# Optimization experiments

Hardware: AMD Instinct MI355X
Metric: run time of the kernel (lower is better)

The kernel has to match this reference:

```python
import jax, jax.numpy as jnp
import numpy as np

NEG_INF = float("-inf")
WINDOW = 5  # window_size in LocalAttention; half = WINDOW // 2 = 2


def setup_inputs() -> dict:
    key = jax.random.key(0)
    kq, kk, kv = jax.random.split(key, 3)
    B, L, H, E = 4, 2048, 8, 64
    queries = jax.random.normal(kq, (B, L, H, E), dtype=jnp.float32)
    keys = jax.random.normal(kk, (B, L, H, E), dtype=jnp.float32)
    values = jax.random.normal(kv, (B, L, H, E), dtype=jnp.float32)
    return {"queries": queries, "keys": keys, "values": values}


def reference(queries, keys, values):
    # queries/keys/values: [B, L, H, E]; dropout is identity (eval mode).
    B, L, H, E = queries.shape
    scale = 1.0 / jnp.sqrt(jnp.asarray(E, dtype=queries.dtype))
    # Shared scores for both branches: [B, H, L, S]
    scores = jnp.einsum("blhe,bshe->bhls", queries, keys)

    # Global (unmasked) branch
    A_global = jax.nn.softmax(scale * scores, axis=-1)

    # Local branch: torch mask allows j in [max(i-2,0), min(i+2,L)) => i-2 <= j <= i+1
    half = WINDOW // 2
    i = jnp.arange(L)[:, None]
    j = jnp.arange(L)[None, :]
    allowed = (j - i >= -half) & (j - i < half)  # [L, L], asymmetric window
    local_scores = jnp.where(allowed, scores, NEG_INF)
    A_local = jax.nn.softmax(scale * local_scores, axis=-1)

    # Sum of the two attention outputs == (A_global + A_local) @ V
    out = jnp.einsum("bhls,bshd->blhd", A_global + A_local, values)
    return out
```

## Files before the change

### kernel.cpp

```cpp
#include <hip/hip_runtime.h>
#include <hip/hip_bf16.h>
#include <stdint.h>


#define LQ 2048
#define HQ 8
#define EQ 64
#define BQ 4
#define BM 64
#define BN 64
#define RS (HQ * EQ)
#define SCALE_LOG2E 0.18033688011112042f
#define NTILE (LQ / BN)
#define TILE_U32 2048
#define IMG_U32 (BQ * HQ * NTILE * TILE_U32)

typedef __attribute__((ext_vector_type(8))) short bf16x8;
typedef __attribute__((ext_vector_type(4))) float f32x4;
typedef __attribute__((ext_vector_type(4))) unsigned int u32x4;
typedef __attribute__((ext_vector_type(2))) unsigned int u32x2;

static __device__ __forceinline__ unsigned int pk2(float lo, float hi) {
    union { float f; unsigned int u; } a, b; a.f = lo; b.f = hi;
    return ((a.u + 0x8000u) >> 16) | ((b.u + 0x8000u) & 0xffff0000u);
}
static __device__ __forceinline__ float fexp2(float x) {
    float r;
    asm volatile("v_exp_f32 %0, %1\n\ts_nop 1" : "=v"(r) : "v"(x));
    return r;
}
static __device__ __forceinline__ void gload16(const uint32_t* g, void* l) {
    __builtin_amdgcn_global_load_lds(
        (const __attribute__((address_space(1))) unsigned int*)g,
        (__attribute__((address_space(3))) unsigned int*)l, 16, 0, 0);
}

__global__ __launch_bounds__(256) void prepack_kernel(
    const float* __restrict__ K, const float* __restrict__ V,
    uint32_t* __restrict__ Kimg, uint32_t* __restrict__ Vimg)
{
    const int tid = threadIdx.x;
    const int jc  = blockIdx.x;
    const int bh  = blockIdx.y;
    const int b   = bh >> 3;
    const int h   = bh & 7;
    const int j0  = jc * BN;
    const float* Kbh = K + (size_t)b * LQ * RS + h * EQ;
    const float* Vbh = V + (size_t)b * LQ * RS + h * EQ;
    uint32_t* Kt = Kimg + (size_t)(bh * NTILE + jc) * TILE_U32;
    uint32_t* Vt = Vimg + (size_t)(bh * NTILE + jc) * TILE_U32;

    #pragma unroll
    for (int it = 0; it < 2; ++it) {
        int t2 = tid + it * 256;
        int jr = t2 >> 3, eo = t2 & 7;
        const float* src = Kbh + (size_t)(j0 + jr) * RS + eo * 8;
        float4 a  = *(const float4*)src;
        float4 bv = *(const float4*)(src + 4);
        u32x4 p;
        p.x = pk2(a.x, a.y);   p.y = pk2(a.z, a.w);
        p.z = pk2(bv.x, bv.y); p.w = pk2(bv.z, bv.w);
        *(u32x4*)&Kt[jr * 32 + ((eo ^ (jr & 7)) << 2)] = p;
    }
    #pragma unroll
    for (int it = 0; it < 2; ++it) {
        int t2 = tid + it * 256;
        int e = t2 & 63, jo = t2 >> 6;
        const float* src = Vbh + (size_t)(j0 + jo * 8) * RS + e;
        float v0 = src[0 * RS], v1 = src[1 * RS], v2 = src[2 * RS], v3 = src[3 * RS];
        float v4 = src[4 * RS], v5 = src[5 * RS], v6 = src[6 * RS], v7 = src[7 * RS];
        u32x4 p;
        p.x = pk2(v0, v1); p.y = pk2(v2, v3);
        p.z = pk2(v4, v5); p.w = pk2(v6, v7);
        *(u32x4*)&Vt[e * 32 + ((jo ^ (e & 7)) << 2)] = p;
    }
}

__global__ __launch_bounds__(128, 2) void hybrid_attn_v5(
    const float* __restrict__ Q, const float* __restrict__ K,
    const float* __restrict__ V, const uint32_t* __restrict__ Kimg,
    const uint32_t* __restrict__ Vimg, float* __restrict__ O)
{
    __shared__ unsigned short KV[8192];
    __shared__ unsigned short Pt[2][2048];
    __shared__ float sloc[BM][4];

    const int tid  = threadIdx.x;
    const int wave = tid >> 6;
    const int lane = tid & 63;
    const int c    = lane & 15;
    const int g    = lane >> 4;
    const int qt   = blockIdx.x;
    const int bh   = blockIdx.y;
    const int b    = bh >> 3;
    const int h    = bh & 7;
    const int i0   = qt * BM;
    const int c7   = c & 7;
    const int sw3  = c7 << 1;

    const float* Qbh = Q + (size_t)b * LQ * RS + h * EQ;
    const float* Kbh = K + (size_t)b * LQ * RS + h * EQ;
    const float* Vbh = V + (size_t)b * LQ * RS + h * EQ;
    float*       Obh = O + (size_t)b * LQ * RS + h * EQ;

    bf16x8 qf[2][2];
    #pragma unroll
    for (int t = 0; t < 2; ++t) {
        const int iq = i0 + wave * 32 + t * 16 + c;
        const float* qrow = Qbh + (size_t)iq * RS + g * 8;
        #pragma unroll
        for (int f = 0; f < 2; ++f) {
            float4 a  = *(const float4*)(qrow + f * 32);
            float4 bv = *(const float4*)(qrow + f * 32 + 4);
            union { bf16x8 v; unsigned int u[4]; } fr;
            fr.u[0] = pk2(a.x  * SCALE_LOG2E, a.y  * SCALE_LOG2E);
            fr.u[1] = pk2(a.z  * SCALE_LOG2E, a.w  * SCALE_LOG2E);
            fr.u[2] = pk2(bv.x * SCALE_LOG2E, bv.y * SCALE_LOG2E);
            fr.u[3] = pk2(bv.z * SCALE_LOG2E, bv.w * SCALE_LOG2E);
            qf[t][f] = fr.v;
        }
    }

    const int fo0 = c * 64 + ((g ^ c7) << 3);
    const int fo1 = c * 64 + (((4 | g) ^ c7) << 3);

    unsigned short* pw[4];
    #pragma unroll
    for (int n = 0; n < 4; ++n)
        pw[n] = &Pt[wave][c * 64 + ((((n << 2) | g) ^ sw3) << 2)];
    unsigned short* pr0 = &Pt[wave][c * 64 + (((g << 1) ^ sw3) << 2)];
    unsigned short* pr1 = &Pt[wave][c * 64 + (((8 | (g << 1)) ^ sw3) << 2)];

    const uint32_t* kgb = Kimg + (size_t)bh * (NTILE * TILE_U32) + wave * 1024 + lane * 4;
    const uint32_t* vgb = Vimg + (size_t)bh * (NTILE * TILE_U32) + wave * 1024 + lane * 4;

    f32x4 oacc[2][4];
    #pragma unroll
    for (int t = 0; t < 2; ++t)
        #pragma unroll
        for (int eg = 0; eg < 4; ++eg) oacc[t][eg] = (f32x4){0.f, 0.f, 0.f, 0.f};
    float lsum[2] = {0.f, 0.f};

    for (int jc = 0; jc < NTILE; ++jc) {
        __syncthreads();
        const uint32_t* kg = kgb + (size_t)jc * TILE_U32;
        const uint32_t* vg = vgb + (size_t)jc * TILE_U32;
        #pragma unroll
        for (int kk = 0; kk < 4; ++kk)
            gload16(kg + kk * 256, &KV[wave * 2048 + kk * 512]);
        #pragma unroll
        for (int kk = 0; kk < 4; ++kk)
            gload16(vg + kk * 256, &KV[4096 + wave * 2048 + kk * 512]);
        __syncthreads();

        bf16x8 kfr[4][2];
        #pragma unroll
        for (int n = 0; n < 4; ++n) {
            kfr[n][0] = *(const bf16x8*)&KV[n * 1024 + fo0];
            kfr[n][1] = *(const bf16x8*)&KV[n * 1024 + fo1];
        }

        #pragma unroll
        for (int t = 0; t < 2; ++t) {
            f32x4 sf[4];
            #pragma unroll
            for (int n = 0; n < 4; ++n) {
                f32x4 acc = (f32x4){0.f, 0.f, 0.f, 0.f};
                acc = __builtin_amdgcn_mfma_f32_16x16x32_bf16(kfr[n][0], qf[t][0], acc, 0, 0, 0);
                acc = __builtin_amdgcn_mfma_f32_16x16x32_bf16(kfr[n][1], qf[t][1], acc, 0, 0, 0);
                sf[n] = acc;
            }
            float ls = 0.f;
            #pragma unroll
            for (int n = 0; n < 4; ++n) {
                float p0 = fexp2(sf[n][0]);
                float p1 = fexp2(sf[n][1]);
                float p2 = fexp2(sf[n][2]);
                float p3 = fexp2(sf[n][3]);
                ls += (p0 + p1) + (p2 + p3);
                u32x2 pkd;
                pkd.x = pk2(p0, p1);
                pkd.y = pk2(p2, p3);
                *(u32x2*)(pw[n] + t * 1024) = pkd;
            }
            lsum[t] += ls;
        }
        asm volatile("s_waitcnt lgkmcnt(0)" ::: "memory");

        bf16x8 pfr[2][2];
        #pragma unroll
        for (int t = 0; t < 2; ++t) {
            pfr[t][0] = *(const bf16x8*)(pr0 + t * 1024);
            pfr[t][1] = *(const bf16x8*)(pr1 + t * 1024);
        }
        #pragma unroll
        for (int eg = 0; eg < 4; ++eg) {
            bf16x8 v0 = *(const bf16x8*)&KV[4096 + eg * 1024 + fo0];
            bf16x8 v1 = *(const bf16x8*)&KV[4096 + eg * 1024 + fo1];
            #pragma unroll
            for (int t = 0; t < 2; ++t) {
                oacc[t][eg] = __builtin_amdgcn_mfma_f32_16x16x32_bf16(v0, pfr[t][0], oacc[t][eg], 0, 0, 0);
                oacc[t][eg] = __builtin_amdgcn_mfma_f32_16x16x32_bf16(v1, pfr[t][1], oacc[t][eg], 0, 0, 0);
            }
        }
    }

    float linv[2];
    #pragma unroll
    for (int t = 0; t < 2; ++t) {
        float l = lsum[t];
        l += __shfl_xor(l, 16);
        l += __shfl_xor(l, 32);
        linv[t] = 1.0f / l;
    }

    {
        const int br = tid >> 1;
        const int i  = i0 + br;
        const float* qrow = Qbh + (size_t)i * RS;
        #pragma unroll
        for (int halfj = 0; halfj < 2; ++halfj) {
            const int jj = (tid & 1) * 2 + halfj;
            const int j  = i - 2 + jj;
            float s = -INFINITY;
            if (j >= 0 && j < LQ) {
                const float* krow = Kbh + (size_t)j * RS;
                float acc = 0.f;
                #pragma unroll
                for (int e = 0; e < 64; e += 4) {
                    float4 qa = *(const float4*)(qrow + e);
                    float4 ka = *(const float4*)(krow + e);
                    acc = fmaf(qa.x, ka.x, acc); acc = fmaf(qa.y, ka.y, acc);
                    acc = fmaf(qa.z, ka.z, acc); acc = fmaf(qa.w, ka.w, acc);
                }
                s = 0.125f * acc;
            }
            sloc[br][jj] = s;
        }
    }
    __syncthreads();

    #pragma unroll
    for (int t = 0; t < 2; ++t) {
        const int row = wave * 32 + t * 16 + c;
        const int i   = i0 + row;
        float s0 = sloc[row][0], s1 = sloc[row][1], s2 = sloc[row][2], s3 = sloc[row][3];
        float mx = fmaxf(fmaxf(s0, s1), fmaxf(s2, s3));
        float w0 = expf(s0 - mx), w1 = expf(s1 - mx);
        float w2 = expf(s2 - mx), w3 = expf(s3 - mx);
        float inv = 1.0f / (w0 + w1 + w2 + w3);
        w0 *= inv; w1 *= inv; w2 *= inv; w3 *= inv;
        const float li = linv[t];
        float* orow = Obh + (size_t)i * RS;
        #pragma unroll
        for (int eg = 0; eg < 4; ++eg) {
            const int e0 = eg * 16 + g * 4;
            float v0 = oacc[t][eg][0] * li;
            float v1 = oacc[t][eg][1] * li;
            float v2 = oacc[t][eg][2] * li;
            float v3 = oacc[t][eg][3] * li;
            if (w0 > 0.f) {
                float4 vv = *(const float4*)(Vbh + (size_t)(i - 2) * RS + e0);
                v0 = fmaf(w0, vv.x, v0); v1 = fmaf(w0, vv.y, v1);
                v2 = fmaf(w0, vv.z, v2); v3 = fmaf(w0, vv.w, v3);
            }
            if (w1 > 0.f) {
                float4 vv = *(const float4*)(Vbh + (size_t)(i - 1) * RS + e0);
                v0 = fmaf(w1, vv.x, v0); v1 = fmaf(w1, vv.y, v1);
                v2 = fmaf(w1, vv.z, v2); v3 = fmaf(w1, vv.w, v3);
            }
            {
                float4 vv = *(const float4*)(Vbh + (size_t)i * RS + e0);
                v0 = fmaf(w2, vv.x, v0); v1 = fmaf(w2, vv.y, v1);
                v2 = fmaf(w2, vv.z, v2); v3 = fmaf(w2, vv.w, v3);
            }
            if (w3 > 0.f) {
                float4 vv = *(const float4*)(Vbh + (size_t)(i + 1) * RS + e0);
                v0 = fmaf(w3, vv.x, v0); v1 = fmaf(w3, vv.y, v1);
                v2 = fmaf(w3, vv.z, v2); v3 = fmaf(w3, vv.w, v3);
            }
            float4 outv; outv.x = v0; outv.y = v1; outv.z = v2; outv.w = v3;
            *(float4*)(orow + e0) = outv;
        }
    }
}

__global__ __launch_bounds__(256) void hybrid_attn_fb(
    const float* __restrict__ Q, const float* __restrict__ K,
    const float* __restrict__ V, float* __restrict__ O)
{
    __shared__ unsigned short Ks[64 * 64];
    __shared__ unsigned short Vt[64 * 64];
    __shared__ unsigned short Ps[4][16 * 64];
    __shared__ float sloc[BM][4];

    const int tid  = threadIdx.x;
    const int wave = tid >> 6;
    const int lane = tid & 63;
    const int c    = lane & 15;
    const int g    = lane >> 4;
    const int qt   = blockIdx.x;
    const int bh   = blockIdx.y;
    const int b    = bh >> 3;
    const int h    = bh & 7;
    const int i0   = qt * BM;

    const float* Qbh = Q + (size_t)b * LQ * RS + h * EQ;
    const float* Kbh = K + (size_t)b * LQ * RS + h * EQ;
    const float* Vbh = V + (size_t)b * LQ * RS + h * EQ;
    float*       Obh = O + (size_t)b * LQ * RS + h * EQ;

    bf16x8 qf[2];
    {
        const int iA = i0 + wave * 16 + c;
        const float* qrow = Qbh + (size_t)iA * RS + g * 8;
        #pragma unroll
        for (int f = 0; f < 2; ++f) {
            float4 a  = *(const float4*)(qrow + f * 32);
            float4 bv = *(const float4*)(qrow + f * 32 + 4);
            union { bf16x8 v; unsigned int u[4]; } fr;
            fr.u[0] = pk2(a.x  * SCALE_LOG2E, a.y  * SCALE_LOG2E);
            fr.u[1] = pk2(a.z  * SCALE_LOG2E, a.w  * SCALE_LOG2E);
            fr.u[2] = pk2(bv.x * SCALE_LOG2E, bv.y * SCALE_LOG2E);
            fr.u[3] = pk2(bv.z * SCALE_LOG2E, bv.w * SCALE_LOG2E);
            qf[f] = fr.v;
        }
    }

    int kfo[4][2], vfo[4][2], pfo[2], pso[4][4];
    #pragma unroll
    for (int n = 0; n < 4; ++n)
        #pragma unroll
        for (int f = 0; f < 2; ++f)
            kfo[n][f] = (n * 16 + c) * 64 + ((((f << 2) | g) ^ (c & 7)) << 3);
    #pragma unroll
    for (int eg = 0; eg < 4; ++eg)
        #pragma unroll
        for (int kh = 0; kh < 2; ++kh)
            vfo[eg][kh] = (eg * 16 + c) * 64 + ((((kh << 2) | g) ^ (c & 7)) << 3);
    #pragma unroll
    for (int kh = 0; kh < 2; ++kh)
        pfo[kh] = c * 64 + ((((kh << 2) | g) ^ (c & 7)) << 3);
    #pragma unroll
    for (int r = 0; r < 4; ++r) {
        const int row = g * 4 + r;
        #pragma unroll
        for (int n = 0; n < 4; ++n) {
            const int col = n * 16 + c;
            pso[r][n] = row * 64 + ((((col >> 3) ^ (row & 7)) << 3) | (col & 7));
        }
    }

    f32x4 oacc[4];
    #pragma unroll
    for (int eg = 0; eg < 4; ++eg) oacc[eg] = (f32x4){0.f, 0.f, 0.f, 0.f};
    float l_r[4] = {0.f, 0.f, 0.f, 0.f};

    for (int j0 = 0; j0 < LQ; j0 += BN) {
        __syncthreads();
        #pragma unroll
        for (int it = 0; it < 2; ++it) {
            int t2 = tid + it * 256;
            int jr = t2 >> 3, eo = t2 & 7;
            const float* src = Kbh + (size_t)(j0 + jr) * RS + eo * 8;
            float4 a  = *(const float4*)src;
            float4 bv = *(const float4*)(src + 4);
            u32x4 p;
            p.x = pk2(a.x, a.y);   p.y = pk2(a.z, a.w);
            p.z = pk2(bv.x, bv.y); p.w = pk2(bv.z, bv.w);
            *(u32x4*)&Ks[jr * 64 + ((eo ^ (jr & 7)) << 3)] = p;
        }
        #pragma unroll
        for (int it = 0; it < 2; ++it) {
            int t2 = tid + it * 256;
            int e = t2 & 63, jo = t2 >> 6;
            const float* src = Vbh + (size_t)(j0 + jo * 8) * RS + e;
            float v0 = src[0 * RS], v1 = src[1 * RS], v2 = src[2 * RS], v3 = src[3 * RS];
            float v4 = src[4 * RS], v5 = src[5 * RS], v6 = src[6 * RS], v7 = src[7 * RS];
            u32x4 p;
            p.x = pk2(v0, v1); p.y = pk2(v2, v3);
            p.z = pk2(v4, v5); p.w = pk2(v6, v7);
            *(u32x4*)&Vt[e * 64 + ((jo ^ (e & 7)) << 3)] = p;
        }
        __syncthreads();

        f32x4 sf[4];
        #pragma unroll
        for (int n = 0; n < 4; ++n) {
            bf16x8 k0 = *(const bf16x8*)&Ks[kfo[n][0]];
            bf16x8 k1 = *(const bf16x8*)&Ks[kfo[n][1]];
            f32x4 acc = (f32x4){0.f, 0.f, 0.f, 0.f};
            acc = __builtin_amdgcn_mfma_f32_16x16x32_bf16(qf[0], k0, acc, 0, 0, 0);
            acc = __builtin_amdgcn_mfma_f32_16x16x32_bf16(qf[1], k1, acc, 0, 0, 0);
            sf[n] = acc;
        }
        #pragma unroll
        for (int r = 0; r < 4; ++r) {
            float p0 = fexp2(sf[0][r]);
            float p1 = fexp2(sf[1][r]);
            float p2 = fexp2(sf[2][r]);
            float p3 = fexp2(sf[3][r]);
            l_r[r] += (p0 + p1) + (p2 + p3);
            Ps[wave][pso[r][0]] = (unsigned short)(pk2(p0, 0.f) & 0xffff);
            Ps[wave][pso[r][1]] = (unsigned short)(pk2(p1, 0.f) & 0xffff);
            Ps[wave][pso[r][2]] = (unsigned short)(pk2(p2, 0.f) & 0xffff);
            Ps[wave][pso[r][3]] = (unsigned short)(pk2(p3, 0.f) & 0xffff);
        }
        asm volatile("s_waitcnt lgkmcnt(0)" ::: "memory");

        bf16x8 pf0 = *(const bf16x8*)&Ps[wave][pfo[0]];
        bf16x8 pf1 = *(const bf16x8*)&Ps[wave][pfo[1]];
        #pragma unroll
        for (int eg = 0; eg < 4; ++eg) {
            bf16x8 v0 = *(const bf16x8*)&Vt[vfo[eg][0]];
            bf16x8 v1 = *(const bf16x8*)&Vt[vfo[eg][1]];
            oacc[eg] = __builtin_amdgcn_mfma_f32_16x16x32_bf16(pf0, v0, oacc[eg], 0, 0, 0);
            oacc[eg] = __builtin_amdgcn_mfma_f32_16x16x32_bf16(pf1, v1, oacc[eg], 0, 0, 0);
        }
    }

    #pragma unroll
    for (int r = 0; r < 4; ++r) {
        float l = l_r[r];
        l += __shfl_xor(l, 1);
        l += __shfl_xor(l, 2);
        l += __shfl_xor(l, 4);
        l += __shfl_xor(l, 8);
        l_r[r] = 1.0f / l;
    }

    {
        const int br = tid >> 2;
        const int jj = tid & 3;
        const int i  = i0 + br;
        const int j  = i - 2 + jj;
        float s = -INFINITY;
        if (j >= 0 && j < LQ) {
            const float* qrow = Qbh + (size_t)i * RS;
            const float* krow = Kbh + (size_t)j * RS;
            float acc = 0.f;
            #pragma unroll
            for (int e = 0; e < 64; e += 4) {
                float4 qa = *(const float4*)(qrow + e);
                float4 ka = *(const float4*)(krow + e);
                acc = fmaf(qa.x, ka.x, acc); acc = fmaf(qa.y, ka.y, acc);
                acc = fmaf(qa.z, ka.z, acc); acc = fmaf(qa.w, ka.w, acc);
            }
            s = 0.125f * acc;
        }
        sloc[br][jj] = s;
    }
    __syncthreads();

    #pragma unroll
    for (int r = 0; r < 4; ++r) {
        const int row = wave * 16 + g * 4 + r;
        const int i   = i0 + row;
        float s0 = sloc[row][0], s1 = sloc[row][1], s2 = sloc[row][2], s3 = sloc[row][3];
        float mx = fmaxf(fmaxf(s0, s1), fmaxf(s2, s3));
        float w0 = expf(s0 - mx), w1 = expf(s1 - mx);
        float w2 = expf(s2 - mx), w3 = expf(s3 - mx);
        float inv = 1.0f / (w0 + w1 + w2 + w3);
        w0 *= inv; w1 *= inv; w2 *= inv; w3 *= inv;
        const float li = l_r[r];
        float* orow = Obh + (size_t)i * RS;
        #pragma unroll
        for (int eg = 0; eg < 4; ++eg) {
            const int e = eg * 16 + c;
            float val = oacc[eg][r] * li;
            if (w0 > 0.f) val += w0 * Vbh[(size_t)(i - 2) * RS + e];
            if (w1 > 0.f) val += w1 * Vbh[(size_t)(i - 1) * RS + e];
            if (w2 > 0.f) val += w2 * Vbh[(size_t)(i    ) * RS + e];
            if (w3 > 0.f) val += w3 * Vbh[(size_t)(i + 1) * RS + e];
            orow[e] = val;
        }
    }
}

extern "C" void kernel_launch(void* const* d_in, const int* in_sizes, int n_in,
                              void* d_out, int out_size, void* d_ws, size_t ws_size,
                              hipStream_t stream) {
    (void)in_sizes; (void)n_in; (void)out_size;
    const float* Q = (const float*)d_in[0];
    const float* K = (const float*)d_in[1];
    const float* V = (const float*)d_in[2];
    float* O = (float*)d_out;
    const size_t need = (size_t)2 * IMG_U32 * 4;
    if (ws_size >= need) {
        uint32_t* Kimg = (uint32_t*)d_ws;
        uint32_t* Vimg = Kimg + IMG_U32;
        hipLaunchKernelGGL(prepack_kernel, dim3(NTILE, BQ * HQ), dim3(256), 0, stream,
                           K, V, Kimg, Vimg);
        hipLaunchKernelGGL(hybrid_attn_v5, dim3(LQ / BM, BQ * HQ), dim3(128), 0, stream,
                           Q, K, V, Kimg, Vimg, O);
    } else {
        hipLaunchKernelGGL(hybrid_attn_fb, dim3(LQ / BM, BQ * HQ), dim3(256), 0, stream,
                           Q, K, V, O);
    }
}
```

Measured before the change: 163.6 us.

## Coalesce V prepack via LDS transpose and remap grid for XCD locality

The V prepack now reads rows with coalesced float4 loads into a padded LDS tile, converts to bf16 and transposes there, replacing the strided scalar column gathers. The main attention kernel uses a 1D grid whose block index is remapped so that consecutive blocks land on different batch-head pairs, likely so each XCD's L2 holds fewer distinct K/V images. The P bf16 conversion uses a simpler single-value helper. The changes add an LDS barrier in the prepack and depend on the hardware dispatch order for the locality benefit.

```diff
diff --git a/kernel.cpp b/kernel.cpp
--- a/kernel.cpp
+++ b/kernel.cpp
@@ -20,6 +20,10 @@
 typedef __attribute__((ext_vector_type(4))) unsigned int u32x4;
 typedef __attribute__((ext_vector_type(2))) unsigned int u32x2;
 
+static __device__ __forceinline__ unsigned int f2bf(float f) {
+    union { float f; unsigned int u; } c; c.f = f;
+    return (c.u + 0x8000u) >> 16;
+}
 static __device__ __forceinline__ unsigned int pk2(float lo, float hi) {
     union { float f; unsigned int u; } a, b; a.f = lo; b.f = hi;
     return ((a.u + 0x8000u) >> 16) | ((b.u + 0x8000u) & 0xffff0000u);
@@ -39,6 +43,8 @@
     const float* __restrict__ K, const float* __restrict__ V,
     uint32_t* __restrict__ Kimg, uint32_t* __restrict__ Vimg)
 {
+    __shared__ unsigned short vt[64 * 72];
+
     const int tid = threadIdx.x;
     const int jc  = blockIdx.x;
     const int bh  = blockIdx.y;
@@ -62,21 +68,33 @@
         p.z = pk2(bv.x, bv.y); p.w = pk2(bv.z, bv.w);
         *(u32x4*)&Kt[jr * 32 + ((eo ^ (jr & 7)) << 2)] = p;
     }
+
+    {
+        const int jr = tid >> 2;
+        const int e0 = (tid & 3) * 16;
+        const float* src = Vbh + (size_t)(j0 + jr) * RS + e0;
+        #pragma unroll
+        for (int q = 0; q < 4; ++q) {
+            float4 a = *(const float4*)(src + q * 4);
+            const int e = e0 + q * 4;
+            vt[(e + 0) * 72 + jr] = (unsigned short)f2bf(a.x);
+            vt[(e + 1) * 72 + jr] = (unsigned short)f2bf(a.y);
+            vt[(e + 2) * 72 + jr] = (unsigned short)f2bf(a.z);
+            vt[(e + 3) * 72 + jr] = (unsigned short)f2bf(a.w);
+        }
+    }
+    __syncthreads();
+
     #pragma unroll
     for (int it = 0; it < 2; ++it) {
-        int t2 = tid + it * 256;
-        int e = t2 & 63, jo = t2 >> 6;
-        const float* src = Vbh + (size_t)(j0 + jo * 8) * RS + e;
-        float v0 = src[0 * RS], v1 = src[1 * RS], v2 = src[2 * RS], v3 = src[3 * RS];
-        float v4 = src[4 * RS], v5 = src[5 * RS], v6 = src[6 * RS], v7 = src[7 * RS];
-        u32x4 p;
-        p.x = pk2(v0, v1); p.y = pk2(v2, v3);
-        p.z = pk2(v4, v5); p.w = pk2(v6, v7);
+        const int i  = tid + it * 256;
+        const int e  = i >> 3, jo = i & 7;
+        u32x4 p = *(const u32x4*)&vt[e * 72 + jo * 8];
         *(u32x4*)&Vt[e * 32 + ((jo ^ (e & 7)) << 2)] = p;
     }
 }
 
-__global__ __launch_bounds__(128, 2) void hybrid_attn_v5(
+__global__ __launch_bounds__(128, 2) void hybrid_attn_v7(
     const float* __restrict__ Q, const float* __restrict__ K,
     const float* __restrict__ V, const uint32_t* __restrict__ Kimg,
     const uint32_t* __restrict__ Vimg, float* __restrict__ O)
@@ -90,8 +108,9 @@
     const int lane = tid & 63;
     const int c    = lane & 15;
     const int g    = lane >> 4;
-    const int qt   = blockIdx.x;
-    const int bh   = blockIdx.y;
+    const int id   = blockIdx.x;
+    const int bh   = (id & 7) * 4 + ((id >> 3) & 3);
+    const int qt   = id >> 5;
     const int b    = bh >> 3;
     const int h    = bh & 7;
     const int i0   = qt * BM;
@@ -401,10 +420,10 @@
             float p2 = fexp2(sf[2][r]);
             float p3 = fexp2(sf[3][r]);
             l_r[r] += (p0 + p1) + (p2 + p3);
-            Ps[wave][pso[r][0]] = (unsigned short)(pk2(p0, 0.f) & 0xffff);
-            Ps[wave][pso[r][1]] = (unsigned short)(pk2(p1, 0.f) & 0xffff);
-            Ps[wave][pso[r][2]] = (unsigned short)(pk2(p2, 0.f) & 0xffff);
-            Ps[wave][pso[r][3]] = (unsigned short)(pk2(p3, 0.f) & 0xffff);
+            Ps[wave][pso[r][0]] = (unsigned short)f2bf(p0);
+            Ps[wave][pso[r][1]] = (unsigned short)f2bf(p1);
+            Ps[wave][pso[r][2]] = (unsigned short)f2bf(p2);
+            Ps[wave][pso[r][3]] = (unsigned short)f2bf(p3);
         }
         asm volatile("s_waitcnt lgkmcnt(0)" ::: "memory");
 
@@ -491,7 +510,7 @@
         uint32_t* Vimg = Kimg + IMG_U32;
         hipLaunchKernelGGL(prepack_kernel, dim3(NTILE, BQ * HQ), dim3(256), 0, stream,
                            K, V, Kimg, Vimg);
-        hipLaunchKernelGGL(hybrid_attn_v5, dim3(LQ / BM, BQ * HQ), dim3(128), 0, stream,
+        hipLaunchKernelGGL(hybrid_attn_v7, dim3((LQ / BM) * BQ * HQ), dim3(128), 0, stream,
                            Q, K, V, Kimg, Vimg, O);
     } else {
         hipLaunchKernelGGL(hybrid_attn_fb, dim3(LQ / BM, BQ * HQ), dim3(256), 0, stream,
```

Measured after the change: 162.7 us. No clear change (-0.5%).
